# Optimization experiments

Measured on AMD Instinct MI355X. Metric: run time of the kernel, lower is better.

Reference implementation:

```python
import jax, jax.numpy as jnp
import numpy as np
import math

B, N, F = 4, 4096, 64
NEG_SLOPE = 0.01


def _leaky_relu(x):
    return jnp.where(x >= 0, x, NEG_SLOPE * x)


def setup_inputs() -> dict:
    key = jax.random.key(0)
    k1, k2, k3, k4, k5 = jax.random.split(key, 5)
    Q = jax.random.normal(k1, (B, N, F, 2), dtype=jnp.float32)
    K = jax.random.normal(k2, (B, N, F, 2), dtype=jnp.float32)
    V = jax.random.normal(k3, (B, N, F, 2), dtype=jnp.float32)
    W_att = jax.random.normal(k4, (F, F), dtype=jnp.float32) / math.sqrt(F)
    b_att = jax.random.normal(k5, (F,), dtype=jnp.float32) * 0.01
    return {"Q": Q, "K": K, "V": V, "W_att": W_att, "b_att": b_att}


def reference(Q, K, V, W_att, b_att):
    # Split complex components: last axis is (real, imag)
    Qr, Qi = Q[..., 0], Q[..., 1]
    Kr, Ki = K[..., 0], K[..., 1]
    Vr, Vi = V[..., 0], V[..., 1]

    n = Q.shape[1]
    scale = 1.0 / math.sqrt(n)  # num_nodes == N

    # Complex scores = Q @ K^T (no conjugation, as in torch einsum on complex)
    sr = (jnp.einsum('bik,bjk->bij', Qr, Kr) - jnp.einsum('bik,bjk->bij', Qi, Ki)) * scale
    si = (jnp.einsum('bik,bjk->bij', Qr, Ki) + jnp.einsum('bik,bjk->bij', Qi, Kr)) * scale

    # Causal mask: positions j > i are masked out (contribute zero weight)
    causal = jnp.tril(jnp.ones((n, n), dtype=bool))  # [N, N], True = keep
    wr = jnp.where(causal, _leaky_relu(sr), 0.0)
    wi = jnp.where(causal, _leaky_relu(si), 0.0)

    # Attention-weighted values (real weights with real V, imag with imag V)
    out_r = jnp.einsum('bij,bjf->bif', wr, Vr)
    out_i = jnp.einsum('bij,bjf->bif', wi, Vi)

    # att_map: shared linear layer
    out_r = out_r @ W_att.T + b_att
    out_i = out_i @ W_att.T + b_att

    return jnp.stack([out_r, out_i], axis=-1)  # [B, N, F, 2]
```

## Files before the change

kernel.cpp:

```cpp
#include <hip/hip_runtime.h>

#define NB 4
#define NN 4096
#define NF 64

typedef __attribute__((ext_vector_type(8))) short bf16x8;
typedef __attribute__((ext_vector_type(4))) float f32x4;

union S8 { unsigned short u[8]; bf16x8 v; };

__device__ __forceinline__ unsigned short f2bf(float x) {
    unsigned int uu = __builtin_bit_cast(unsigned int, x);
    uu += 0x7fffu + ((uu >> 16) & 1u);
    return (unsigned short)(uu >> 16);
}

__global__ void prep_qk(const float* __restrict__ Q, const float* __restrict__ K,
                        short* __restrict__ QF, short* __restrict__ KF) {
    int tid = blockIdx.x * 256 + threadIdx.x;
    int sel = tid >> 17;
    int r   = tid & 0x1FFFF;
    int l  = r & 63;
    int c  = (r >> 6) & 1;
    int rg = (r >> 7) & 255;
    int b  = r >> 15;
    const float* src = sel ? K : Q;
    short*       dst = sel ? KF : QF;

    int row = rg * 16 + (l & 15);
    int k0  = c * 32 + (l >> 4) * 8;
    const float4* s4 = (const float4*)src;
    int base4 = (b * NN + row) * 32 + (k0 >> 1);

    S8 ar, ai;
    #pragma unroll
    for (int m = 0; m < 4; ++m) {
        float4 f = s4[base4 + m];
        ar.u[2 * m]     = f2bf(f.x);
        ar.u[2 * m + 1] = f2bf(f.z);
        ai.u[2 * m]     = f2bf(f.y);
        ai.u[2 * m + 1] = f2bf(f.w);
    }
    int cid0 = ((b * 256 + rg) * 2 + c) * 2;
    *(bf16x8*)(dst + (cid0 + 0) * 512 + l * 8) = ar.v;
    *(bf16x8*)(dst + (cid0 + 1) * 512 + l * 8) = ai.v;
}

__global__ void prep_v(const float* __restrict__ V, short* __restrict__ VF) {
    int r = blockIdx.x * 256 + threadIdx.x;
    int l  = r & 63;
    int c  = (r >> 6) & 1;
    int ft = (r >> 7) & 3;
    int jt = (r >> 9) & 63;
    int b  = (r >> 15) & 3;

    int f  = ft * 16 + (l & 15);
    int j0 = jt * 64 + c * 32 + (l >> 4) * 8;
    const float2* s2 = (const float2*)V;

    S8 ar, ai;
    #pragma unroll
    for (int e = 0; e < 8; ++e) {
        float2 g = s2[(b * NN + j0 + e) * 64 + f];
        ar.u[e] = f2bf(g.x);
        ai.u[e] = f2bf(g.y);
    }
    int cid0 = (((b * 64 + jt) * 4 + ft) * 2 + c) * 2;
    *(bf16x8*)(VF + (cid0 + 0) * 512 + l * 8) = ar.v;
    *(bf16x8*)(VF + (cid0 + 1) * 512 + l * 8) = ai.v;
}

__global__ void prep_w(const float* __restrict__ W, short* __restrict__ WF) {
    int r = blockIdx.x * 256 + threadIdx.x;
    if (r >= 512) return;
    int l  = r & 63;
    int c  = (r >> 6) & 1;
    int ft = r >> 7;
    int row = ft * 16 + (l & 15);
    int k0  = c * 32 + (l >> 4) * 8;
    const float* sp = W + row * 64 + k0;
    S8 a;
    #pragma unroll
    for (int e = 0; e < 8; ++e) a.u[e] = f2bf(sp[e]);
    *(bf16x8*)(WF + ((ft * 2 + c) * 64 + l) * 8) = a.v;
}

__global__ __launch_bounds__(256, 2)
void attn_main(const short* __restrict__ QF, const short* __restrict__ KF,
               const short* __restrict__ VF, const short* __restrict__ WF,
               const float* __restrict__ batt, float* __restrict__ out) {
    __shared__ __align__(16) unsigned short wbuf[4][2048];

    int m  = blockIdx.x;
    int u  = m & 255;
    int b  = u >> 6;
    int vt = u & 63;
    int sp = m >> 8;
    int it = sp ? (63 - vt) : vt;
    int ntiles = it + 1;
    int halfc  = (ntiles + 1) >> 1;
    int jt0 = sp ? halfc : 0;
    int jt1 = sp ? ntiles : halfc;

    int w   = threadIdx.x >> 6;
    int l   = threadIdx.x & 63;
    int r16 = l & 15;
    int lb  = l >> 4;

    const f32x4 z = {0.f, 0.f, 0.f, 0.f};
    const float SCALE = 1.0f / 64.0f;

    bf16x8 qf[2][2];
    {
        int rg = it * 4 + w;
        #pragma unroll
        for (int c = 0; c < 2; ++c)
            #pragma unroll
            for (int ch = 0; ch < 2; ++ch)
                qf[c][ch] = *(const bf16x8*)(QF + (((b * 256 + rg) * 2 + c) * 2 + ch) * 512 + l * 8);
    }

    f32x4 o[4][2];
    #pragma unroll
    for (int ft = 0; ft < 4; ++ft) { o[ft][0] = z; o[ft][1] = z; }

    unsigned short* wb = wbuf[w];

    for (int jt = jt0; jt < jt1; ++jt) {
        bool diag = (jt == it);
        #pragma unroll
        for (int ct = 0; ct < 4; ++ct) {
            bf16x8 kf[2][2];
            int rg = jt * 4 + ct;
            #pragma unroll
            for (int c = 0; c < 2; ++c)
                #pragma unroll
                for (int ch = 0; ch < 2; ++ch)
                    kf[c][ch] = *(const bf16x8*)(KF + (((b * 256 + rg) * 2 + c) * 2 + ch) * 512 + l * 8);

            f32x4 t1 = __builtin_amdgcn_mfma_f32_16x16x32_bf16(qf[0][0], kf[0][0], z, 0, 0, 0);
            t1 = __builtin_amdgcn_mfma_f32_16x16x32_bf16(qf[1][0], kf[1][0], t1, 0, 0, 0);
            f32x4 t2 = __builtin_amdgcn_mfma_f32_16x16x32_bf16(qf[0][1], kf[0][1], z, 0, 0, 0);
            t2 = __builtin_amdgcn_mfma_f32_16x16x32_bf16(qf[1][1], kf[1][1], t2, 0, 0, 0);
            f32x4 si = __builtin_amdgcn_mfma_f32_16x16x32_bf16(qf[0][0], kf[0][1], z, 0, 0, 0);
            si = __builtin_amdgcn_mfma_f32_16x16x32_bf16(qf[1][0], kf[1][1], si, 0, 0, 0);
            si = __builtin_amdgcn_mfma_f32_16x16x32_bf16(qf[0][1], kf[0][0], si, 0, 0, 0);
            si = __builtin_amdgcn_mfma_f32_16x16x32_bf16(qf[1][1], kf[1][0], si, 0, 0, 0);

            int cH  = ct >> 1;
            int lb2 = ((ct & 1) << 1) | (r16 >> 3);
            int e   = r16 & 7;
            int base_r = (cH * 2 + 0) * 512 + lb2 * 128 + lb * 32 + e;
            int base_i = (cH * 2 + 1) * 512 + lb2 * 128 + lb * 32 + e;
            #pragma unroll
            for (int reg = 0; reg < 4; ++reg) {
                float sr = (t1[reg] - t2[reg]) * SCALE;
                float sv = si[reg] * SCALE;
                float wr = sr >= 0.f ? sr : 0.01f * sr;
                float wi = sv >= 0.f ? sv : 0.01f * sv;
                if (diag) {
                    int ig = w * 16 + lb * 4 + reg;
                    int jg = ct * 16 + r16;
                    if (jg > ig) { wr = 0.f; wi = 0.f; }
                }
                wb[base_r + reg * 8] = f2bf(wr);
                wb[base_i + reg * 8] = f2bf(wi);
            }
        }
        __builtin_amdgcn_sched_barrier(0);

        bf16x8 wfr[2][2];
        #pragma unroll
        for (int c = 0; c < 2; ++c)
            #pragma unroll
            for (int ch = 0; ch < 2; ++ch)
                wfr[c][ch] = *(const bf16x8*)(wb + (c * 2 + ch) * 512 + l * 8);
        __builtin_amdgcn_sched_barrier(0);

        #pragma unroll
        for (int ft = 0; ft < 4; ++ft) {
            #pragma unroll
            for (int ch = 0; ch < 2; ++ch) {
                int cid0 = (((b * 64 + jt) * 4 + ft) * 2) * 2 + ch;
                bf16x8 v0 = *(const bf16x8*)(VF + cid0 * 512 + l * 8);
                bf16x8 v1 = *(const bf16x8*)(VF + (cid0 + 2) * 512 + l * 8);
                o[ft][ch] = __builtin_amdgcn_mfma_f32_16x16x32_bf16(wfr[0][ch], v0, o[ft][ch], 0, 0, 0);
                o[ft][ch] = __builtin_amdgcn_mfma_f32_16x16x32_bf16(wfr[1][ch], v1, o[ft][ch], 0, 0, 0);
            }
        }
        __builtin_amdgcn_sched_barrier(0);
    }

    __builtin_amdgcn_sched_barrier(0);
    #pragma unroll
    for (int ft = 0; ft < 4; ++ft) {
        int cH  = ft >> 1;
        int lb2 = ((ft & 1) << 1) | (r16 >> 3);
        int e   = r16 & 7;
        #pragma unroll
        for (int ch = 0; ch < 2; ++ch) {
            int base = (cH * 2 + ch) * 512 + lb2 * 128 + lb * 32 + e;
            #pragma unroll
            for (int reg = 0; reg < 4; ++reg)
                wb[base + reg * 8] = f2bf(o[ft][ch][reg]);
        }
    }
    __builtin_amdgcn_sched_barrier(0);

    bf16x8 of[2][2];
    #pragma unroll
    for (int c = 0; c < 2; ++c)
        #pragma unroll
        for (int ch = 0; ch < 2; ++ch)
            of[c][ch] = *(const bf16x8*)(wb + (c * 2 + ch) * 512 + l * 8);

    int ibase = b * NN + it * 64 + w * 16 + lb * 4;
    #pragma unroll
    for (int ft2 = 0; ft2 < 4; ++ft2) {
        bf16x8 wa0 = *(const bf16x8*)(WF + ((ft2 * 2 + 0) * 64 + l) * 8);
        bf16x8 wa1 = *(const bf16x8*)(WF + ((ft2 * 2 + 1) * 64 + l) * 8);
        float bb = (sp == 0) ? batt[ft2 * 16 + r16] : 0.f;
        #pragma unroll
        for (int ch = 0; ch < 2; ++ch) {
            f32x4 acc = __builtin_amdgcn_mfma_f32_16x16x32_bf16(of[0][ch], wa0, z, 0, 0, 0);
            acc = __builtin_amdgcn_mfma_f32_16x16x32_bf16(of[1][ch], wa1, acc, 0, 0, 0);
            #pragma unroll
            for (int reg = 0; reg < 4; ++reg) {
                int idx = ((ibase + reg) * 64 + ft2 * 16 + r16) * 2 + ch;
                atomicAdd(out + idx, acc[reg] + bb);
            }
        }
    }
}

extern "C" void kernel_launch(void* const* d_in, const int* in_sizes, int n_in,
                              void* d_out, int out_size, void* d_ws, size_t ws_size,
                              hipStream_t stream) {
    const float* Q  = (const float*)d_in[0];
    const float* K  = (const float*)d_in[1];
    const float* V  = (const float*)d_in[2];
    const float* W  = (const float*)d_in[3];
    const float* bA = (const float*)d_in[4];
    float* out = (float*)d_out;

    short* QF = (short*)d_ws;
    short* KF = QF + 2097152;
    short* VF = KF + 2097152;
    short* WF = VF + 2097152;

    hipMemsetAsync(d_out, 0, (size_t)out_size * sizeof(float), stream);
    prep_qk<<<1024, 256, 0, stream>>>(Q, K, QF, KF);
    prep_v<<<512, 256, 0, stream>>>(V, VF);
    prep_w<<<2, 256, 0, stream>>>(W, WF);
    attn_main<<<512, 256, 0, stream>>>(QF, KF, VF, WF, bA, out);
}
```

Before: 216.3 us.

## Balance causal tiles with fixed chunks and merge prep kernels with zeroing

```diff
diff --git a/kernel.cpp b/kernel.cpp
--- a/kernel.cpp
+++ b/kernel.cpp
@@ -3,6 +3,8 @@
 #define NB 4
 #define NN 4096
 #define NF 64
+#define TSTEP 8
+#define BLKS_PER_B 260
 
 typedef __attribute__((ext_vector_type(8))) short bf16x8;
 typedef __attribute__((ext_vector_type(4))) float f32x4;
@@ -15,92 +17,99 @@
     return (unsigned short)(uu >> 16);
 }
 
-__global__ void prep_qk(const float* __restrict__ Q, const float* __restrict__ K,
-                        short* __restrict__ QF, short* __restrict__ KF) {
+__global__ __launch_bounds__(256)
+void prep_all(const float* __restrict__ Q, const float* __restrict__ K,
+              const float* __restrict__ V, const float* __restrict__ W,
+              short* __restrict__ QF, short* __restrict__ KF,
+              short* __restrict__ VF, short* __restrict__ WF,
+              float* __restrict__ out) {
     int tid = blockIdx.x * 256 + threadIdx.x;
-    int sel = tid >> 17;
-    int r   = tid & 0x1FFFF;
-    int l  = r & 63;
-    int c  = (r >> 6) & 1;
-    int rg = (r >> 7) & 255;
-    int b  = r >> 15;
-    const float* src = sel ? K : Q;
-    short*       dst = sel ? KF : QF;
-
-    int row = rg * 16 + (l & 15);
-    int k0  = c * 32 + (l >> 4) * 8;
-    const float4* s4 = (const float4*)src;
-    int base4 = (b * NN + row) * 32 + (k0 >> 1);
-
-    S8 ar, ai;
-    #pragma unroll
-    for (int m = 0; m < 4; ++m) {
-        float4 f = s4[base4 + m];
-        ar.u[2 * m]     = f2bf(f.x);
-        ar.u[2 * m + 1] = f2bf(f.z);
-        ai.u[2 * m]     = f2bf(f.y);
-        ai.u[2 * m + 1] = f2bf(f.w);
+
+    if (tid < 262144) {
+        int sel = tid >> 17;
+        int r   = tid & 0x1FFFF;
+        int l  = r & 63;
+        int c  = (r >> 6) & 1;
+        int rg = (r >> 7) & 255;
+        int b  = r >> 15;
+        const float* src = sel ? K : Q;
+        short*       dst = sel ? KF : QF;
+
+        int row = rg * 16 + (l & 15);
+        int k0  = c * 32 + (l >> 4) * 8;
+        const float4* s4 = (const float4*)src;
+        int base4 = (b * NN + row) * 32 + (k0 >> 1);
+
+        S8 ar, ai;
+        #pragma unroll
+        for (int m = 0; m < 4; ++m) {
+            float4 f = s4[base4 + m];
+            ar.u[2 * m]     = f2bf(f.x);
+            ar.u[2 * m + 1] = f2bf(f.z);
+            ai.u[2 * m]     = f2bf(f.y);
+            ai.u[2 * m + 1] = f2bf(f.w);
+        }
+        int cid0 = ((b * 256 + rg) * 2 + c) * 2;
+        *(bf16x8*)(dst + (cid0 + 0) * 512 + l * 8) = ar.v;
+        *(bf16x8*)(dst + (cid0 + 1) * 512 + l * 8) = ai.v;
+    } else if (tid < 393216) {
+        int r = tid - 262144;
+        int l  = r & 63;
+        int c  = (r >> 6) & 1;
+        int ft = (r >> 7) & 3;
+        int jt = (r >> 9) & 63;
+        int b  = (r >> 15) & 3;
+
+        int f  = ft * 16 + (l & 15);
+        int j0 = jt * 64 + c * 32 + (l >> 4) * 8;
+        const float2* s2 = (const float2*)V;
+
+        S8 ar, ai;
+        #pragma unroll
+        for (int e = 0; e < 8; ++e) {
+            float2 g = s2[(b * NN + j0 + e) * 64 + f];
+            ar.u[e] = f2bf(g.x);
+            ai.u[e] = f2bf(g.y);
+        }
+        int cid0 = (((b * 64 + jt) * 4 + ft) * 2 + c) * 2;
+        *(bf16x8*)(VF + (cid0 + 0) * 512 + l * 8) = ar.v;
+        *(bf16x8*)(VF + (cid0 + 1) * 512 + l * 8) = ai.v;
+    } else if (tid < 393728) {
+        int r = tid - 393216;
+        int l  = r & 63;
+        int c  = (r >> 6) & 1;
+        int ft = r >> 7;
+        int row = ft * 16 + (l & 15);
+        int k0  = c * 32 + (l >> 4) * 8;
+        const float* sp = W + row * 64 + k0;
+        S8 a;
+        #pragma unroll
+        for (int e = 0; e < 8; ++e) a.u[e] = f2bf(sp[e]);
+        *(bf16x8*)(WF + ((ft * 2 + c) * 64 + l) * 8) = a.v;
+    } else {
+        int r = tid - 393728;
+        float4 zz = {0.f, 0.f, 0.f, 0.f};
+        ((float4*)out)[r] = zz;
     }
-    int cid0 = ((b * 256 + rg) * 2 + c) * 2;
-    *(bf16x8*)(dst + (cid0 + 0) * 512 + l * 8) = ar.v;
-    *(bf16x8*)(dst + (cid0 + 1) * 512 + l * 8) = ai.v;
-}
-
-__global__ void prep_v(const float* __restrict__ V, short* __restrict__ VF) {
-    int r = blockIdx.x * 256 + threadIdx.x;
-    int l  = r & 63;
-    int c  = (r >> 6) & 1;
-    int ft = (r >> 7) & 3;
-    int jt = (r >> 9) & 63;
-    int b  = (r >> 15) & 3;
-
-    int f  = ft * 16 + (l & 15);
-    int j0 = jt * 64 + c * 32 + (l >> 4) * 8;
-    const float2* s2 = (const float2*)V;
-
-    S8 ar, ai;
-    #pragma unroll
-    for (int e = 0; e < 8; ++e) {
-        float2 g = s2[(b * NN + j0 + e) * 64 + f];
-        ar.u[e] = f2bf(g.x);
-        ai.u[e] = f2bf(g.y);
-    }
-    int cid0 = (((b * 64 + jt) * 4 + ft) * 2 + c) * 2;
-    *(bf16x8*)(VF + (cid0 + 0) * 512 + l * 8) = ar.v;
-    *(bf16x8*)(VF + (cid0 + 1) * 512 + l * 8) = ai.v;
-}
-
-__global__ void prep_w(const float* __restrict__ W, short* __restrict__ WF) {
-    int r = blockIdx.x * 256 + threadIdx.x;
-    if (r >= 512) return;
-    int l  = r & 63;
-    int c  = (r >> 6) & 1;
-    int ft = r >> 7;
-    int row = ft * 16 + (l & 15);
-    int k0  = c * 32 + (l >> 4) * 8;
-    const float* sp = W + row * 64 + k0;
-    S8 a;
-    #pragma unroll
-    for (int e = 0; e < 8; ++e) a.u[e] = f2bf(sp[e]);
-    *(bf16x8*)(WF + ((ft * 2 + c) * 64 + l) * 8) = a.v;
-}
-
-__global__ __launch_bounds__(256, 2)
+}
+
+__device__ __forceinline__ int tri_inv(int g) {
+    int it = (int)((__builtin_sqrtf(8.0f * (float)g + 1.0f) - 1.0f) * 0.5f);
+    while ((it + 1) * (it + 2) / 2 <= g) ++it;
+    while (it * (it + 1) / 2 > g) --it;
+    return it;
+}
+
+__global__ __launch_bounds__(256, 4)
 void attn_main(const short* __restrict__ QF, const short* __restrict__ KF,
                const short* __restrict__ VF, const short* __restrict__ WF,
                const float* __restrict__ batt, float* __restrict__ out) {
     __shared__ __align__(16) unsigned short wbuf[4][2048];
 
-    int m  = blockIdx.x;
-    int u  = m & 255;
-    int b  = u >> 6;
-    int vt = u & 63;
-    int sp = m >> 8;
-    int it = sp ? (63 - vt) : vt;
-    int ntiles = it + 1;
-    int halfc  = (ntiles + 1) >> 1;
-    int jt0 = sp ? halfc : 0;
-    int jt1 = sp ? ntiles : halfc;
+    int bid = blockIdx.x;
+    int b   = bid / BLKS_PER_B;
+    int g   = (bid % BLKS_PER_B) * TSTEP;
+    int gend = g + TSTEP;
 
     int w   = threadIdx.x >> 6;
     int l   = threadIdx.x & 63;
@@ -109,127 +118,134 @@
 
     const f32x4 z = {0.f, 0.f, 0.f, 0.f};
     const float SCALE = 1.0f / 64.0f;
-
-    bf16x8 qf[2][2];
-    {
-        int rg = it * 4 + w;
+    unsigned short* wb = wbuf[w];
+
+    while (g < gend) {
+        int it   = tri_inv(g);
+        int base = it * (it + 1) / 2;
+        int jt0  = g - base;
+        int cnt  = min(gend - g, it + 1 - jt0);
+        int jt1  = jt0 + cnt;
+
+        bf16x8 qf[2][2];
+        {
+            int rg = it * 4 + w;
+            #pragma unroll
+            for (int c = 0; c < 2; ++c)
+                #pragma unroll
+                for (int ch = 0; ch < 2; ++ch)
+                    qf[c][ch] = *(const bf16x8*)(QF + (((b * 256 + rg) * 2 + c) * 2 + ch) * 512 + l * 8);
+        }
+
+        f32x4 o[4][2];
+        #pragma unroll
+        for (int ft = 0; ft < 4; ++ft) { o[ft][0] = z; o[ft][1] = z; }
+
+        for (int jt = jt0; jt < jt1; ++jt) {
+            bool diag = (jt == it);
+            #pragma unroll
+            for (int ct = 0; ct < 4; ++ct) {
+                bf16x8 kf[2][2];
+                int rg = jt * 4 + ct;
+                #pragma unroll
+                for (int c = 0; c < 2; ++c)
+                    #pragma unroll
+                    for (int ch = 0; ch < 2; ++ch)
+                        kf[c][ch] = *(const bf16x8*)(KF + (((b * 256 + rg) * 2 + c) * 2 + ch) * 512 + l * 8);
+
+                f32x4 t1 = __builtin_amdgcn_mfma_f32_16x16x32_bf16(qf[0][0], kf[0][0], z, 0, 0, 0);
+                t1 = __builtin_amdgcn_mfma_f32_16x16x32_bf16(qf[1][0], kf[1][0], t1, 0, 0, 0);
+                f32x4 t2 = __builtin_amdgcn_mfma_f32_16x16x32_bf16(qf[0][1], kf[0][1], z, 0, 0, 0);
+                t2 = __builtin_amdgcn_mfma_f32_16x16x32_bf16(qf[1][1], kf[1][1], t2, 0, 0, 0);
+                f32x4 si = __builtin_amdgcn_mfma_f32_16x16x32_bf16(qf[0][0], kf[0][1], z, 0, 0, 0);
+                si = __builtin_amdgcn_mfma_f32_16x16x32_bf16(qf[1][0], kf[1][1], si, 0, 0, 0);
+                si = __builtin_amdgcn_mfma_f32_16x16x32_bf16(qf[0][1], kf[0][0], si, 0, 0, 0);
+                si = __builtin_amdgcn_mfma_f32_16x16x32_bf16(qf[1][1], kf[1][0], si, 0, 0, 0);
+
+                int cH  = ct >> 1;
+                int lb2 = ((ct & 1) << 1) | (r16 >> 3);
+                int e   = r16 & 7;
+                int base_r = (cH * 2 + 0) * 512 + lb2 * 128 + lb * 32 + e;
+                int base_i = (cH * 2 + 1) * 512 + lb2 * 128 + lb * 32 + e;
+                #pragma unroll
+                for (int reg = 0; reg < 4; ++reg) {
+                    float sr = (t1[reg] - t2[reg]) * SCALE;
+                    float sv = si[reg] * SCALE;
+                    float wr = sr >= 0.f ? sr : 0.01f * sr;
+                    float wi = sv >= 0.f ? sv : 0.01f * sv;
+                    if (diag) {
+                        int ig = w * 16 + lb * 4 + reg;
+                        int jg = ct * 16 + r16;
+                        if (jg > ig) { wr = 0.f; wi = 0.f; }
+                    }
+                    wb[base_r + reg * 8] = f2bf(wr);
+                    wb[base_i + reg * 8] = f2bf(wi);
+                }
+            }
+
+            bf16x8 wfr[2][2];
+            #pragma unroll
+            for (int c = 0; c < 2; ++c)
+                #pragma unroll
+                for (int ch = 0; ch < 2; ++ch)
+                    wfr[c][ch] = *(const bf16x8*)(wb + (c * 2 + ch) * 512 + l * 8);
+
+            #pragma unroll
+            for (int ft = 0; ft < 4; ++ft) {
+                #pragma unroll
+                for (int ch = 0; ch < 2; ++ch) {
+                    int cid0 = (((b * 64 + jt) * 4 + ft) * 2) * 2 + ch;
+                    bf16x8 v0 = *(const bf16x8*)(VF + cid0 * 512 + l * 8);
+                    bf16x8 v1 = *(const bf16x8*)(VF + (cid0 + 2) * 512 + l * 8);
+                    o[ft][ch] = __builtin_amdgcn_mfma_f32_16x16x32_bf16(wfr[0][ch], v0, o[ft][ch], 0, 0, 0);
+                    o[ft][ch] = __builtin_amdgcn_mfma_f32_16x16x32_bf16(wfr[1][ch], v1, o[ft][ch], 0, 0, 0);
+                }
+            }
+        }
+
+        #pragma unroll
+        for (int ft = 0; ft < 4; ++ft) {
+            int cH  = ft >> 1;
+            int lb2 = ((ft & 1) << 1) | (r16 >> 3);
+            int e   = r16 & 7;
+            #pragma unroll
+            for (int ch = 0; ch < 2; ++ch) {
+                int bofs = (cH * 2 + ch) * 512 + lb2 * 128 + lb * 32 + e;
+                #pragma unroll
+                for (int reg = 0; reg < 4; ++reg)
+                    wb[bofs + reg * 8] = f2bf(o[ft][ch][reg]);
+            }
+        }
+
+        bf16x8 of[2][2];
         #pragma unroll
         for (int c = 0; c < 2; ++c)
             #pragma unroll
             for (int ch = 0; ch < 2; ++ch)
-                qf[c][ch] = *(const bf16x8*)(QF + (((b * 256 + rg) * 2 + c) * 2 + ch) * 512 + l * 8);
-    }
-
-    f32x4 o[4][2];
-    #pragma unroll
-    for (int ft = 0; ft < 4; ++ft) { o[ft][0] = z; o[ft][1] = z; }
-
-    unsigned short* wb = wbuf[w];
-
-    for (int jt = jt0; jt < jt1; ++jt) {
-        bool diag = (jt == it);
-        #pragma unroll
-        for (int ct = 0; ct < 4; ++ct) {
-            bf16x8 kf[2][2];
-            int rg = jt * 4 + ct;
-            #pragma unroll
-            for (int c = 0; c < 2; ++c)
-                #pragma unroll
-                for (int ch = 0; ch < 2; ++ch)
-                    kf[c][ch] = *(const bf16x8*)(KF + (((b * 256 + rg) * 2 + c) * 2 + ch) * 512 + l * 8);
-
-            f32x4 t1 = __builtin_amdgcn_mfma_f32_16x16x32_bf16(qf[0][0], kf[0][0], z, 0, 0, 0);
-            t1 = __builtin_amdgcn_mfma_f32_16x16x32_bf16(qf[1][0], kf[1][0], t1, 0, 0, 0);
-            f32x4 t2 = __builtin_amdgcn_mfma_f32_16x16x32_bf16(qf[0][1], kf[0][1], z, 0, 0, 0);
-            t2 = __builtin_amdgcn_mfma_f32_16x16x32_bf16(qf[1][1], kf[1][1], t2, 0, 0, 0);
-            f32x4 si = __builtin_amdgcn_mfma_f32_16x16x32_bf16(qf[0][0], kf[0][1], z, 0, 0, 0);
-            si = __builtin_amdgcn_mfma_f32_16x16x32_bf16(qf[1][0], kf[1][1], si, 0, 0, 0);
-            si = __builtin_amdgcn_mfma_f32_16x16x32_bf16(qf[0][1], kf[0][0], si, 0, 0, 0);
-            si = __builtin_amdgcn_mfma_f32_16x16x32_bf16(qf[1][1], kf[1][0], si, 0, 0, 0);
-
-            int cH  = ct >> 1;
-            int lb2 = ((ct & 1) << 1) | (r16 >> 3);
-            int e   = r16 & 7;
-            int base_r = (cH * 2 + 0) * 512 + lb2 * 128 + lb * 32 + e;
-            int base_i = (cH * 2 + 1) * 512 + lb2 * 128 + lb * 32 + e;
-            #pragma unroll
-            for (int reg = 0; reg < 4; ++reg) {
-                float sr = (t1[reg] - t2[reg]) * SCALE;
-                float sv = si[reg] * SCALE;
-                float wr = sr >= 0.f ? sr : 0.01f * sr;
-                float wi = sv >= 0.f ? sv : 0.01f * sv;
-                if (diag) {
-                    int ig = w * 16 + lb * 4 + reg;
-                    int jg = ct * 16 + r16;
-                    if (jg > ig) { wr = 0.f; wi = 0.f; }
+                of[c][ch] = *(const bf16x8*)(wb + (c * 2 + ch) * 512 + l * 8);
+
+        bool whole = (jt0 == 0) && (jt1 == it + 1);
+        bool addb  = (jt0 == 0);
+        int ibase = b * NN + it * 64 + w * 16 + lb * 4;
+        #pragma unroll
+        for (int ft2 = 0; ft2 < 4; ++ft2) {
+            bf16x8 wa0 = *(const bf16x8*)(WF + ((ft2 * 2 + 0) * 64 + l) * 8);
+            bf16x8 wa1 = *(const bf16x8*)(WF + ((ft2 * 2 + 1) * 64 + l) * 8);
+            float bb = addb ? batt[ft2 * 16 + r16] : 0.f;
+            #pragma unroll
+            for (int ch = 0; ch < 2; ++ch) {
+                f32x4 acc = __builtin_amdgcn_mfma_f32_16x16x32_bf16(of[0][ch], wa0, z, 0, 0, 0);
+                acc = __builtin_amdgcn_mfma_f32_16x16x32_bf16(of[1][ch], wa1, acc, 0, 0, 0);
+                #pragma unroll
+                for (int reg = 0; reg < 4; ++reg) {
+                    int idx = ((ibase + reg) * 64 + ft2 * 16 + r16) * 2 + ch;
+                    if (whole) out[idx] = acc[reg] + bb;
+                    else       atomicAdd(out + idx, acc[reg] + bb);
                 }
-                wb[base_r + reg * 8] = f2bf(wr);
-                wb[base_i + reg * 8] = f2bf(wi);
-            }
-        }
-        __builtin_amdgcn_sched_barrier(0);
-
-        bf16x8 wfr[2][2];
-        #pragma unroll
-        for (int c = 0; c < 2; ++c)
-            #pragma unroll
-            for (int ch = 0; ch < 2; ++ch)
-                wfr[c][ch] = *(const bf16x8*)(wb + (c * 2 + ch) * 512 + l * 8);
-        __builtin_amdgcn_sched_barrier(0);
-
-        #pragma unroll
-        for (int ft = 0; ft < 4; ++ft) {
-            #pragma unroll
-            for (int ch = 0; ch < 2; ++ch) {
-                int cid0 = (((b * 64 + jt) * 4 + ft) * 2) * 2 + ch;
-                bf16x8 v0 = *(const bf16x8*)(VF + cid0 * 512 + l * 8);
-                bf16x8 v1 = *(const bf16x8*)(VF + (cid0 + 2) * 512 + l * 8);
-                o[ft][ch] = __builtin_amdgcn_mfma_f32_16x16x32_bf16(wfr[0][ch], v0, o[ft][ch], 0, 0, 0);
-                o[ft][ch] = __builtin_amdgcn_mfma_f32_16x16x32_bf16(wfr[1][ch], v1, o[ft][ch], 0, 0, 0);
-            }
-        }
-        __builtin_amdgcn_sched_barrier(0);
-    }
-
-    __builtin_amdgcn_sched_barrier(0);
-    #pragma unroll
-    for (int ft = 0; ft < 4; ++ft) {
-        int cH  = ft >> 1;
-        int lb2 = ((ft & 1) << 1) | (r16 >> 3);
-        int e   = r16 & 7;
-        #pragma unroll
-        for (int ch = 0; ch < 2; ++ch) {
-            int base = (cH * 2 + ch) * 512 + lb2 * 128 + lb * 32 + e;
-            #pragma unroll
-            for (int reg = 0; reg < 4; ++reg)
-                wb[base + reg * 8] = f2bf(o[ft][ch][reg]);
-        }
-    }
-    __builtin_amdgcn_sched_barrier(0);
-
-    bf16x8 of[2][2];
-    #pragma unroll
-    for (int c = 0; c < 2; ++c)
-        #pragma unroll
-        for (int ch = 0; ch < 2; ++ch)
-            of[c][ch] = *(const bf16x8*)(wb + (c * 2 + ch) * 512 + l * 8);
-
-    int ibase = b * NN + it * 64 + w * 16 + lb * 4;
-    #pragma unroll
-    for (int ft2 = 0; ft2 < 4; ++ft2) {
-        bf16x8 wa0 = *(const bf16x8*)(WF + ((ft2 * 2 + 0) * 64 + l) * 8);
-        bf16x8 wa1 = *(const bf16x8*)(WF + ((ft2 * 2 + 1) * 64 + l) * 8);
-        float bb = (sp == 0) ? batt[ft2 * 16 + r16] : 0.f;
-        #pragma unroll
-        for (int ch = 0; ch < 2; ++ch) {
-            f32x4 acc = __builtin_amdgcn_mfma_f32_16x16x32_bf16(of[0][ch], wa0, z, 0, 0, 0);
-            acc = __builtin_amdgcn_mfma_f32_16x16x32_bf16(of[1][ch], wa1, acc, 0, 0, 0);
-            #pragma unroll
-            for (int reg = 0; reg < 4; ++reg) {
-                int idx = ((ibase + reg) * 64 + ft2 * 16 + r16) * 2 + ch;
-                atomicAdd(out + idx, acc[reg] + bb);
-            }
-        }
+            }
+        }
+
+        g += cnt;
     }
 }
 
@@ -248,9 +264,6 @@
     short* VF = KF + 2097152;
     short* WF = VF + 2097152;
 
-    hipMemsetAsync(d_out, 0, (size_t)out_size * sizeof(float), stream);
-    prep_qk<<<1024, 256, 0, stream>>>(Q, K, QF, KF);
-    prep_v<<<512, 256, 0, stream>>>(V, VF);
-    prep_w<<<2, 256, 0, stream>>>(W, WF);
-    attn_main<<<512, 256, 0, stream>>>(QF, KF, VF, WF, bA, out);
-}
+    prep_all<<<3586, 256, 0, stream>>>(Q, K, V, W, QF, KF, VF, WF, out);
+    attn_main<<<NB * BLKS_PER_B, 256, 0, stream>>>(QF, KF, VF, WF, bA, out);
+}
```

Result: faster. 198.3 us (-8.3%).
